# Performance work log

Hardware: AMD Instinct MI355X
Metric: run time of the kernel (lower is better)

## Reference

```python
import jax, jax.numpy as jnp
import numpy as np

B, T, C = 2, 2048, 1024
H = 16
D = C // H  # head_dim = 64


def setup_inputs() -> dict:
    key = jax.random.key(0)
    k1, k2, k3, k4, k5 = jax.random.split(key, 5)
    s = 1.0 / np.sqrt(C)
    return {
        "x": jax.random.normal(k1, (B, T, C), dtype=jnp.float32),
        "w_qkv": jax.random.normal(k2, (C, 3 * C), dtype=jnp.float32) * s,
        "b_qkv": jax.random.normal(k3, (3 * C,), dtype=jnp.float32) * 0.01,
        "w_out": jax.random.normal(k4, (C, C), dtype=jnp.float32) * s,
        "b_out": jax.random.normal(k5, (C,), dtype=jnp.float32) * 0.01,
    }


def reference(x, w_qkv, b_qkv, w_out, b_out):
    Bx, Tx, Cx = x.shape
    qkv = x @ w_qkv + b_qkv                      # [B,T,3C]
    qkv = qkv.reshape(Bx, Tx, 3, H, D)
    q, k, v = qkv[:, :, 0], qkv[:, :, 1], qkv[:, :, 2]  # [B,T,H,D]
    # [B,H,T,T] scores with scaling
    scores = jnp.einsum("bqhd,bkhd->bhqk", q, k) / np.sqrt(D).astype(np.float32)
    causal = jnp.tril(jnp.ones((Tx, Tx), dtype=bool))
    scores = jnp.where(causal[None, None], scores, -jnp.inf)
    attn = jax.nn.softmax(scores, axis=-1)
    out = jnp.einsum("bhqk,bkhd->bqhd", attn, v).reshape(Bx, Tx, Cx)
    return out @ w_out + b_out
```

## Files before the change

### kernel.cpp

```cpp
#include <hip/hip_runtime.h>
#include <stdint.h>

typedef unsigned short u16;
typedef __attribute__((ext_vector_type(8))) short bfrag;
typedef __attribute__((ext_vector_type(4))) short bfrag4;
typedef __attribute__((ext_vector_type(4))) float f32x4;

#define MFMA_BF16 __builtin_amdgcn_mfma_f32_16x16x32_bf16

static constexpr int Bc = 2;
static constexpr int Tc = 2048;
static constexpr int Cc = 1024;
static constexpr int Hc = 16;
static constexpr int Dc = 64;
static constexpr int N2 = 2 * Cc;

__device__ __forceinline__ u16 f2bf(float f) {
    union { unsigned int i; float f; } v; v.f = f;
    unsigned int u = v.i;
    u += 0x7fffu + ((u >> 16) & 1u);
    return (u16)(u >> 16);
}
__device__ __forceinline__ unsigned int fbits(float f) {
    union { unsigned int i; float f; } v; v.f = f; return v.i;
}
__device__ __forceinline__ unsigned int pack_bf2(float hi, float lo) {
    return __builtin_amdgcn_perm(fbits(hi), fbits(lo), 0x07060302u);
}

#if __has_builtin(__builtin_amdgcn_mfma_f32_16x16x16bf16_1k)
__device__ __forceinline__ f32x4 MFMA16(bfrag4 a, bfrag4 b, f32x4 c) {
    return __builtin_amdgcn_mfma_f32_16x16x16bf16_1k(a, b, c, 0, 0, 0);
}
#elif __has_builtin(__builtin_amdgcn_mfma_f32_16x16x16_bf16)
__device__ __forceinline__ f32x4 MFMA16(bfrag4 a, bfrag4 b, f32x4 c) {
    return __builtin_amdgcn_mfma_f32_16x16x16_bf16(a, b, c, 0, 0, 0);
}
#else
__device__ __forceinline__ f32x4 MFMA16(bfrag4 a, bfrag4 b, f32x4 c) {
    bfrag a8 = {a[0], a[1], a[2], a[3], 0, 0, 0, 0};
    bfrag b8 = {b[0], b[1], b[2], b[3], 0, 0, 0, 0};
    return MFMA_BF16(a8, b8, c, 0, 0, 0);
}
#endif

__device__ __forceinline__ void async_load16(const u16* g, u16* lds) {
    __builtin_amdgcn_global_load_lds(
        (const __attribute__((address_space(1))) unsigned int*)g,
        (__attribute__((address_space(3))) unsigned int*)lds, 16, 0, 0);
}

__global__ __launch_bounds__(256) void prep(
    const float* __restrict__ x, const float* __restrict__ w_qkv,
    const float* __restrict__ w_out, u16* __restrict__ xb,
    u16* __restrict__ WqkvT, u16* __restrict__ WoutT) {
    __shared__ u16 tile[32][33];
    const int blk = blockIdx.x, tid = threadIdx.x;
    if (blk < 4096) {
        const int i = (blk * 256 + tid) * 4;
        const float4 v = *(const float4*)(x + i);
        ushort4 o;
        o.x = f2bf(v.x); o.y = f2bf(v.y); o.z = f2bf(v.z); o.w = f2bf(v.w);
        *(ushort4*)(xb + i) = o;
        return;
    }
    const int tx = tid & 31, ty = tid >> 5;
    const float* in; u16* out; int rows, cols, c0, r0;
    if (blk < 4096 + 3072) {
        const int t = blk - 4096;
        in = w_qkv; out = WqkvT; rows = 1024; cols = 3072;
        c0 = (t % 96) * 32; r0 = (t / 96) * 32;
    } else {
        const int t = blk - 7168;
        in = w_out; out = WoutT; rows = 1024; cols = 1024;
        c0 = (t & 31) * 32; r0 = (t >> 5) * 32;
    }
    for (int i = 0; i < 4; i++)
        tile[ty + 8 * i][tx] = f2bf(in[(size_t)(r0 + ty + 8 * i) * cols + c0 + tx]);
    __syncthreads();
    for (int i = 0; i < 4; i++)
        out[(size_t)(c0 + ty + 8 * i) * rows + r0 + tx] = tile[tx][ty + 8 * i];
}

template <int MODE>
__global__ __launch_bounds__(256) void gemm_bt(
    const u16* __restrict__ A, const u16* __restrict__ BT,
    const float* __restrict__ bias, void* __restrict__ out_p,
    u16* __restrict__ Vt, int M, int Nn, int K) {
    constexpr int SELEMS = (MODE == 1) ? 128 * 136 : 4 * 4096;
    __shared__ __align__(16) u16 smem[SELEMS];

    const int tid  = threadIdx.x;
    const int wave = tid >> 6, lane = tid & 63;
    const int quad = lane >> 4, l16 = lane & 15;
    const int wm = wave & 1, wn = wave >> 1;
    const int m0 = blockIdx.y * 128, n0 = blockIdx.x * 128;

    f32x4 acc[4][4];
    #pragma unroll
    for (int i = 0; i < 4; i++)
        #pragma unroll
        for (int j = 0; j < 4; j++)
            acc[i][j] = (f32x4){0.f, 0.f, 0.f, 0.f};

    const int rloc = 2 * (lane >> 3) + ((lane >> 2) & 1);
    const int cg   = ((lane & 3) ^ ((lane >> 3) & 3)) * 8;
    const int rk   = (l16 >> 1) & 3;
    const int rodd = (l16 & 1) * 32;

    const int T = K >> 5;
    #define STAGE(t, bsel)                                                      \
        {                                                                       \
            const int k0_ = (t) << 5;                                           \
            const int ao_ = (bsel) * 4096;                                      \
            _Pragma("unroll")                                                   \
            for (int j = 0; j < 2; j++) {                                       \
                const int R0 = wave * 32 + j * 16;                              \
                async_load16(A  + (size_t)(m0 + R0 + rloc) * K + k0_ + cg,      \
                             smem + ao_ + R0 * 32);                             \
                async_load16(BT + (size_t)(n0 + R0 + rloc) * K + k0_ + cg,      \
                             smem + 8192 + ao_ + R0 * 32);                      \
            }                                                                   \
        }

    STAGE(0, 0);
    for (int t = 0; t < T; t++) {
        __syncthreads();
        if (t + 1 < T) STAGE(t + 1, (t + 1) & 1);
        const u16* Ab = smem + (t & 1) * 4096;
        const u16* Bb = smem + 8192 + (t & 1) * 4096;
        bfrag af[4], bf[4];
        #pragma unroll
        for (int mt = 0; mt < 4; mt++) {
            const int r = wm * 64 + mt * 16 + l16;
            af[mt] = *(const bfrag*)(Ab + (r >> 1) * 64 + rodd + (quad ^ rk) * 8);
        }
        #pragma unroll
        for (int nt = 0; nt < 4; nt++) {
            const int r = wn * 64 + nt * 16 + l16;
            bf[nt] = *(const bfrag*)(Bb + (r >> 1) * 64 + rodd + (quad ^ rk) * 8);
        }
        #pragma unroll
        for (int mt = 0; mt < 4; mt++)
            #pragma unroll
            for (int nt = 0; nt < 4; nt++)
                acc[mt][nt] = MFMA_BF16(af[mt], bf[nt], acc[mt][nt], 0, 0, 0);
    }
    #undef STAGE

    if (MODE == 1 && n0 >= 2048) {
        __syncthreads();
        #pragma unroll
        for (int nt = 0; nt < 4; nt++) {
            const int ln = wn * 64 + nt * 16 + l16;
            const float bv = bias[n0 + ln];
            u16* col = smem + ln * 136;
            #pragma unroll
            for (int mt = 0; mt < 4; mt++) {
                const int lmb = wm * 64 + mt * 16 + quad * 4;
                #pragma unroll
                for (int r = 0; r < 4; r++)
                    col[lmb + r] = f2bf(acc[mt][nt][r] + bv);
            }
        }
        __syncthreads();
        const int bb = m0 >> 11, t0 = m0 & 2047;
        const int h0 = (n0 - 2048) >> 6;
        const int dl = tid >> 1;
        const int th = (tid & 1) * 64;
        u16* dst = Vt + ((size_t)(bb * Hc + h0 + (dl >> 6)) * Dc + (dl & 63)) * Tc
                      + t0 + th;
        const u16* srcr = smem + dl * 136 + th;
        #pragma unroll
        for (int c = 0; c < 8; c++)
            *(uint4*)(dst + c * 8) = *(const uint4*)(srcr + c * 8);
    } else {
        #pragma unroll
        for (int nt = 0; nt < 4; nt++) {
            const int gn = n0 + wn * 64 + nt * 16 + l16;
            const float bv = bias[gn];
            #pragma unroll
            for (int mt = 0; mt < 4; mt++) {
                #pragma unroll
                for (int r = 0; r < 4; r++) {
                    const int gm = m0 + wm * 64 + mt * 16 + quad * 4 + r;
                    if (MODE == 1)
                        ((u16*)out_p)[(size_t)gm * Nn + gn] = f2bf(acc[mt][nt][r] + bv);
                    else
                        ((float*)out_p)[(size_t)gm * Nn + gn] = acc[mt][nt][r] + bv;
                }
            }
        }
    }
}

__global__ __launch_bounds__(256, 4) void attn_kernel(
    const u16* __restrict__ QKp, const u16* __restrict__ Vt,
    u16* __restrict__ Ob) {
    __shared__ __align__(16) u16 KsF[2][64 * 64];
    __shared__ __align__(16) u16 VsF[2][64 * 64];

    const int tid  = threadIdx.x;
    const int wave = tid >> 6, lane = tid & 63;
    const int quad = lane >> 4, l16 = lane & 15;

    const int bh = blockIdx.x & 31;
    const int jq = 31 - (blockIdx.x >> 5);
    const int b = bh >> 4, h = bh & 15;
    const u16* Qp = QKp + (size_t)b * Tc * N2 + h * Dc;
    const u16* Kp = Qp + Cc;
    const u16* Vp = Vt + (size_t)bh * Dc * Tc;

    const int qw = jq * 64 + wave * 16;

    const int row8 = lane >> 3;
    const int swz  = ((lane & 7) ^ row8) * 8;
    const int pk0 = ((quad)     ^ (l16 & 7)) * 8;
    const int pk1 = ((quad + 4) ^ (l16 & 7)) * 8;

    bfrag qf0, qf1;
    {
        const u16* qp = Qp + (size_t)(qw + l16) * N2 + quad * 8;
        qf0 = *(const bfrag*)qp;
        qf1 = *(const bfrag*)(qp + 32);
    }

    float l_i = 0.f;
    f32x4 oacc[4];
    #pragma unroll
    for (int g = 0; g < 4; g++) oacc[g] = (f32x4){0.f, 0.f, 0.f, 0.f};

    #define STAGEKV(t, bsel)                                                    \
        {                                                                       \
            const int k0_ = (t) * 64;                                           \
            _Pragma("unroll")                                                   \
            for (int j = 0; j < 2; j++) {                                       \
                const int rr = wave * 16 + j * 8;                               \
                const int gr = rr + row8;                                       \
                async_load16(Kp + (size_t)(k0_ + gr) * N2 + swz,                \
                             &KsF[bsel][rr * 64]);                              \
                async_load16(Vp + (size_t)gr * Tc + k0_ + swz,                  \
                             &VsF[bsel][rr * 64]);                              \
            }                                                                   \
        }

    STAGEKV(0, 0);
    for (int t = 0; t <= jq; t++) {
        __syncthreads();
        if (t < jq) STAGEKV(t + 1, (t + 1) & 1);
        const u16* Kb = KsF[t & 1];
        const u16* Vb = VsF[t & 1];

        f32x4 s[4];
        #pragma unroll
        for (int g = 0; g < 4; g++) {
            const u16* kb = Kb + (g * 16 + l16) * 64;
            bfrag kf0 = *(const bfrag*)(kb + pk0);
            bfrag kf1 = *(const bfrag*)(kb + pk1);
            f32x4 z = (f32x4){0.f, 0.f, 0.f, 0.f};
            z = MFMA_BF16(kf0, qf0, z, 0, 0, 0);
            z = MFMA_BF16(kf1, qf1, z, 0, 0, 0);
            s[g] = z;
        }

        #pragma unroll
        for (int g = 0; g < 4; g++)
            #pragma unroll
            for (int r = 0; r < 4; r++)
                s[g][r] = __expf(s[g][r] * 0.125f);
        if (t == jq) {
            #pragma unroll
            for (int g = 0; g < 4; g++)
                #pragma unroll
                for (int r = 0; r < 4; r++)
                    if (g * 16 + quad * 4 + r > wave * 16 + l16) s[g][r] = 0.f;
        }
        #pragma unroll
        for (int g = 0; g < 4; g++)
            l_i += s[g][0] + s[g][1] + s[g][2] + s[g][3];

        #pragma unroll
        for (int g = 0; g < 4; g++) {
            union { unsigned int u[2]; bfrag4 v; } pf;
            pf.u[0] = pack_bf2(s[g][1], s[g][0]);
            pf.u[1] = pack_bf2(s[g][3], s[g][2]);
            const int vc = ((2 * g + (quad >> 1)) ^ (l16 & 7)) * 8 + (quad & 1) * 4;
            #pragma unroll
            for (int ng = 0; ng < 4; ng++) {
                const bfrag4 vf = *(const bfrag4*)(Vb + (ng * 16 + l16) * 64 + vc);
                oacc[ng] = MFMA16(vf, pf.v, oacc[ng]);
            }
        }
    }
    #undef STAGEKV

    float rs = l_i;
    rs += __shfl_xor(rs, 16);
    rs += __shfl_xor(rs, 32);
    const float inv = 1.f / rs;
    const int q = qw + l16;
    u16* orow = Ob + (size_t)(b * Tc + q) * Cc + h * Dc + quad * 4;
    #pragma unroll
    for (int ng = 0; ng < 4; ng++) {
        ushort4 o;
        o.x = f2bf(oacc[ng][0] * inv);
        o.y = f2bf(oacc[ng][1] * inv);
        o.z = f2bf(oacc[ng][2] * inv);
        o.w = f2bf(oacc[ng][3] * inv);
        *(ushort4*)(orow + ng * 16) = o;
    }
}

extern "C" void kernel_launch(void* const* d_in, const int* in_sizes, int n_in,
                              void* d_out, int out_size, void* d_ws, size_t ws_size,
                              hipStream_t stream) {
    const float* x     = (const float*)d_in[0];
    const float* w_qkv = (const float*)d_in[1];
    const float* b_qkv = (const float*)d_in[2];
    const float* w_out = (const float*)d_in[3];
    const float* b_out = (const float*)d_in[4];
    float* out = (float*)d_out;
    u16* ws  = (u16*)d_ws;

    u16* xb    = ws;
    u16* WqkvT = xb    + (size_t)4096 * 1024;
    u16* WoutT = WqkvT + (size_t)3072 * 1024;
    u16* QKp   = WoutT + (size_t)1024 * 1024;
    u16* Vt    = QKp   + (size_t)4096 * 2048;
    u16* Ao    = xb;

    prep<<<8192, 256, 0, stream>>>(x, w_qkv, w_out, xb, WqkvT, WoutT);
    gemm_bt<1><<<dim3(3072 / 128, 4096 / 128), 256, 0, stream>>>(
        xb, WqkvT, b_qkv, QKp, Vt, 4096, 2048, 1024);
    attn_kernel<<<1024, 256, 0, stream>>>(QKp, Vt, Ao);
    gemm_bt<0><<<dim3(1024 / 128, 4096 / 128), 256, 0, stream>>>(
        Ao, WoutT, b_out, out, nullptr, 4096, 1024, 1024);
}
```

Measured before the change: 182.9 us.

## Fuse all four stages into one persistent kernel with grid barriers

```diff
diff --git a/kernel.cpp b/kernel.cpp
--- a/kernel.cpp
+++ b/kernel.cpp
@@ -14,6 +14,7 @@
 static constexpr int Hc = 16;
 static constexpr int Dc = 64;
 static constexpr int N2 = 2 * Cc;
+static constexpr int NBLK = 512;
 
 __device__ __forceinline__ u16 f2bf(float f) {
     union { unsigned int i; float f; } v; v.f = f;
@@ -50,51 +51,80 @@
         (__attribute__((address_space(3))) unsigned int*)lds, 16, 0, 0);
 }
 
-__global__ __launch_bounds__(256) void prep(
-    const float* __restrict__ x, const float* __restrict__ w_qkv,
-    const float* __restrict__ w_out, u16* __restrict__ xb,
-    u16* __restrict__ WqkvT, u16* __restrict__ WoutT) {
-    __shared__ u16 tile[32][33];
-    const int blk = blockIdx.x, tid = threadIdx.x;
-    if (blk < 4096) {
-        const int i = (blk * 256 + tid) * 4;
-        const float4 v = *(const float4*)(x + i);
+__device__ __forceinline__ void grid_barrier(unsigned int* bar, unsigned int target) {
+    __syncthreads();
+    if (threadIdx.x == 0) {
+        __threadfence_system();
+        __hip_atomic_fetch_add(bar, 1u, __ATOMIC_RELEASE,
+                               __HIP_MEMORY_SCOPE_SYSTEM);
+        long long t0 = clock64();
+        while (__hip_atomic_load(bar, __ATOMIC_ACQUIRE,
+                                 __HIP_MEMORY_SCOPE_SYSTEM) < target) {
+            __builtin_amdgcn_s_sleep(2);
+            if (clock64() - t0 > 3000000000LL) break;
+        }
+        __threadfence_system();
+    }
+    __syncthreads();
+}
+
+__device__ __forceinline__ int grab(unsigned int* tk, int* s_slot) {
+    __syncthreads();
+    if (threadIdx.x == 0)
+        *s_slot = (int)__hip_atomic_fetch_add(tk, 1u, __ATOMIC_RELAXED,
+                                              __HIP_MEMORY_SCOPE_AGENT);
+    __syncthreads();
+    return *s_slot;
+}
+
+
+__device__ __forceinline__ void prep_body(
+    int blk, int nblk, const float* __restrict__ x,
+    const float* __restrict__ w_qkv, const float* __restrict__ w_out,
+    u16* __restrict__ xb, u16* __restrict__ WqkvT, u16* __restrict__ WoutT,
+    u16* tile) {
+    const int tid = threadIdx.x;
+    const int nthr = nblk * 256;
+    for (int i = blk * 256 + tid; i < 1048576; i += nthr) {
+        const float4 v = *(const float4*)(x + (size_t)i * 4);
         ushort4 o;
         o.x = f2bf(v.x); o.y = f2bf(v.y); o.z = f2bf(v.z); o.w = f2bf(v.w);
-        *(ushort4*)(xb + i) = o;
-        return;
+        *(ushort4*)(xb + (size_t)i * 4) = o;
     }
     const int tx = tid & 31, ty = tid >> 5;
-    const float* in; u16* out; int rows, cols, c0, r0;
-    if (blk < 4096 + 3072) {
-        const int t = blk - 4096;
-        in = w_qkv; out = WqkvT; rows = 1024; cols = 3072;
-        c0 = (t % 96) * 32; r0 = (t / 96) * 32;
-    } else {
-        const int t = blk - 7168;
-        in = w_out; out = WoutT; rows = 1024; cols = 1024;
-        c0 = (t & 31) * 32; r0 = (t >> 5) * 32;
-    }
-    for (int i = 0; i < 4; i++)
-        tile[ty + 8 * i][tx] = f2bf(in[(size_t)(r0 + ty + 8 * i) * cols + c0 + tx]);
-    __syncthreads();
-    for (int i = 0; i < 4; i++)
-        out[(size_t)(c0 + ty + 8 * i) * rows + r0 + tx] = tile[tx][ty + 8 * i];
+    for (int tau = blk; tau < 4096; tau += nblk) {
+        const float* in; u16* outp; int rows, cols, c0, r0;
+        if (tau < 3072) {
+            in = w_qkv; outp = WqkvT; rows = 1024; cols = 3072;
+            c0 = (tau % 96) * 32; r0 = (tau / 96) * 32;
+        } else {
+            const int t2 = tau - 3072;
+            in = w_out; outp = WoutT; rows = 1024; cols = 1024;
+            c0 = (t2 & 31) * 32; r0 = (t2 >> 5) * 32;
+        }
+        __syncthreads();
+        for (int i = 0; i < 4; i++)
+            tile[(ty + 8 * i) * 33 + tx] =
+                f2bf(in[(size_t)(r0 + ty + 8 * i) * cols + c0 + tx]);
+        __syncthreads();
+        for (int i = 0; i < 4; i++)
+            outp[(size_t)(c0 + ty + 8 * i) * rows + r0 + tx] =
+                tile[tx * 33 + ty + 8 * i];
+    }
 }
 
 template <int MODE>
-__global__ __launch_bounds__(256) void gemm_bt(
-    const u16* __restrict__ A, const u16* __restrict__ BT,
+__device__ __forceinline__ void gemm_body(
+    int bx, int by, const u16* __restrict__ A, const u16* __restrict__ BT,
     const float* __restrict__ bias, void* __restrict__ out_p,
-    u16* __restrict__ Vt, int M, int Nn, int K) {
-    constexpr int SELEMS = (MODE == 1) ? 128 * 136 : 4 * 4096;
-    __shared__ __align__(16) u16 smem[SELEMS];
-
+    u16* __restrict__ Vt, int M, int Nn, int K, u16* smem) {
     const int tid  = threadIdx.x;
     const int wave = tid >> 6, lane = tid & 63;
     const int quad = lane >> 4, l16 = lane & 15;
     const int wm = wave & 1, wn = wave >> 1;
-    const int m0 = blockIdx.y * 128, n0 = blockIdx.x * 128;
+    const int m0 = by * 128, n0 = bx * 128;
+
+    __syncthreads();
 
     f32x4 acc[4][4];
     #pragma unroll
@@ -104,7 +134,7 @@
             acc[i][j] = (f32x4){0.f, 0.f, 0.f, 0.f};
 
     const int rloc = 2 * (lane >> 3) + ((lane >> 2) & 1);
-    const int cg   = ((lane & 3) ^ ((lane >> 3) & 3)) * 8;
+    const int cg_  = ((lane & 3) ^ ((lane >> 3) & 3)) * 8;
     const int rk   = (l16 >> 1) & 3;
     const int rodd = (l16 & 1) * 32;
 
@@ -116,9 +146,9 @@
             _Pragma("unroll")                                                   \
             for (int j = 0; j < 2; j++) {                                       \
                 const int R0 = wave * 32 + j * 16;                              \
-                async_load16(A  + (size_t)(m0 + R0 + rloc) * K + k0_ + cg,      \
+                async_load16(A  + (size_t)(m0 + R0 + rloc) * K + k0_ + cg_,     \
                              smem + ao_ + R0 * 32);                             \
-                async_load16(BT + (size_t)(n0 + R0 + rloc) * K + k0_ + cg,      \
+                async_load16(BT + (size_t)(n0 + R0 + rloc) * K + k0_ + cg_,     \
                              smem + 8192 + ao_ + R0 * 32);                      \
             }                                                                   \
         }
@@ -194,18 +224,15 @@
     }
 }
 
-__global__ __launch_bounds__(256, 4) void attn_kernel(
-    const u16* __restrict__ QKp, const u16* __restrict__ Vt,
-    u16* __restrict__ Ob) {
-    __shared__ __align__(16) u16 KsF[2][64 * 64];
-    __shared__ __align__(16) u16 VsF[2][64 * 64];
-
+__device__ __forceinline__ void attn_body(
+    int tau, const u16* __restrict__ QKp, const u16* __restrict__ Vt,
+    u16* __restrict__ Ob, u16* smem) {
     const int tid  = threadIdx.x;
     const int wave = tid >> 6, lane = tid & 63;
     const int quad = lane >> 4, l16 = lane & 15;
 
-    const int bh = blockIdx.x & 31;
-    const int jq = 31 - (blockIdx.x >> 5);
+    const int bh = tau & 31;
+    const int jq = 31 - (tau >> 5);
     const int b = bh >> 4, h = bh & 15;
     const u16* Qp = QKp + (size_t)b * Tc * N2 + h * Dc;
     const u16* Kp = Qp + Cc;
@@ -217,6 +244,8 @@
     const int swz  = ((lane & 7) ^ row8) * 8;
     const int pk0 = ((quad)     ^ (l16 & 7)) * 8;
     const int pk1 = ((quad + 4) ^ (l16 & 7)) * 8;
+
+    __syncthreads();
 
     bfrag qf0, qf1;
     {
@@ -233,14 +262,15 @@
     #define STAGEKV(t, bsel)                                                    \
         {                                                                       \
             const int k0_ = (t) * 64;                                           \
+            const int o_ = (bsel) * 4096;                                       \
             _Pragma("unroll")                                                   \
             for (int j = 0; j < 2; j++) {                                       \
                 const int rr = wave * 16 + j * 8;                               \
                 const int gr = rr + row8;                                       \
                 async_load16(Kp + (size_t)(k0_ + gr) * N2 + swz,                \
-                             &KsF[bsel][rr * 64]);                              \
+                             smem + o_ + rr * 64);                              \
                 async_load16(Vp + (size_t)gr * Tc + k0_ + swz,                  \
-                             &VsF[bsel][rr * 64]);                              \
+                             smem + 8192 + o_ + rr * 64);                       \
             }                                                                   \
         }
 
@@ -248,8 +278,8 @@
     for (int t = 0; t <= jq; t++) {
         __syncthreads();
         if (t < jq) STAGEKV(t + 1, (t + 1) & 1);
-        const u16* Kb = KsF[t & 1];
-        const u16* Vb = VsF[t & 1];
+        const u16* Kb = smem + (t & 1) * 4096;
+        const u16* Vb = smem + 8192 + (t & 1) * 4096;
 
         f32x4 s[4];
         #pragma unroll
@@ -311,6 +341,43 @@
     }
 }
 
+__global__ __launch_bounds__(256, 2) void mega(
+    const float* __restrict__ x, const float* __restrict__ w_qkv,
+    const float* __restrict__ b_qkv, const float* __restrict__ w_out,
+    const float* __restrict__ b_out, float* __restrict__ out,
+    u16* __restrict__ xb, u16* __restrict__ WqkvT, u16* __restrict__ WoutT,
+    u16* __restrict__ QKp, u16* __restrict__ Vt, u16* __restrict__ Ao,
+    unsigned int* __restrict__ ctr) {
+    __shared__ __align__(16) u16 smem[17408];
+    __shared__ int s_slot;
+    unsigned int* bar = ctr;
+
+    prep_body(blockIdx.x, NBLK, x, w_qkv, w_out, xb, WqkvT, WoutT, smem);
+    grid_barrier(bar, NBLK);
+
+    for (;;) {
+        const int t = grab(ctr + 1, &s_slot);
+        if (t >= 768) break;
+        gemm_body<1>(t % 24, t / 24, xb, WqkvT, b_qkv, QKp, Vt,
+                     4096, 2048, 1024, smem);
+    }
+    grid_barrier(bar, 2 * NBLK);
+
+    for (;;) {
+        const int t = grab(ctr + 2, &s_slot);
+        if (t >= 1024) break;
+        attn_body(t, QKp, Vt, Ao, smem);
+    }
+    grid_barrier(bar, 3 * NBLK);
+
+    for (;;) {
+        const int t = grab(ctr + 3, &s_slot);
+        if (t >= 256) break;
+        gemm_body<0>(t & 7, t >> 3, Ao, WoutT, b_out, out, nullptr,
+                     4096, 1024, 1024, smem);
+    }
+}
+
 extern "C" void kernel_launch(void* const* d_in, const int* in_sizes, int n_in,
                               void* d_out, int out_size, void* d_ws, size_t ws_size,
                               hipStream_t stream) {
@@ -328,11 +395,9 @@
     u16* QKp   = WoutT + (size_t)1024 * 1024;
     u16* Vt    = QKp   + (size_t)4096 * 2048;
     u16* Ao    = xb;
-
-    prep<<<8192, 256, 0, stream>>>(x, w_qkv, w_out, xb, WqkvT, WoutT);
-    gemm_bt<1><<<dim3(3072 / 128, 4096 / 128), 256, 0, stream>>>(
-        xb, WqkvT, b_qkv, QKp, Vt, 4096, 2048, 1024);
-    attn_kernel<<<1024, 256, 0, stream>>>(QKp, Vt, Ao);
-    gemm_bt<0><<<dim3(1024 / 128, 4096 / 128), 256, 0, stream>>>(
-        Ao, WoutT, b_out, out, nullptr, 4096, 1024, 1024);
-}
+    unsigned int* ctr = (unsigned int*)(ws + (size_t)24 * 1024 * 1024);
+
+    hipMemsetAsync(ctr, 0, 16, stream);
+    mega<<<NBLK, 256, 0, stream>>>(x, w_qkv, b_qkv, w_out, b_out, out,
+                                   xb, WqkvT, WoutT, QKp, Vt, Ao, ctr);
+}
```

Result: slower. 668.8 us (+265.6%).
